# Optimization experiments

Measured on AMD Instinct MI355X. Metric: run time of the kernel, lower is better.

## Reference

```python
import jax, jax.numpy as jnp
import numpy as np
from jax import lax

DIM, HEADS, DIM_HEAD = 768, 12, 64
INNER = HEADS * DIM_HEAD
DIM_ROT = 32
FH = FW = 32
N = 1 + FH * FW
B = 8


def setup_inputs() -> dict:
    key = jax.random.key(0)
    ks = jax.random.split(key, 8)
    s = 0.02
    return {
        "x": jax.random.normal(ks[0], (B, N, DIM), jnp.float32),
        "sin": jax.random.normal(ks[1], (N - 1, DIM_ROT), jnp.float32),
        "cos": jax.random.normal(ks[2], (N - 1, DIM_ROT), jnp.float32),
        "ln_g": jnp.ones((DIM,), jnp.float32),
        "ln_b": jnp.zeros((DIM,), jnp.float32),
        "dw_w": jax.random.normal(ks[3], (DIM, 1, 5, 5), jnp.float32) * s,
        "pw_w": jax.random.normal(ks[4], (INNER, DIM, 1, 1), jnp.float32) * s,
        "kv_w": jax.random.normal(ks[5], (DIM, 2 * INNER), jnp.float32) * s,
        "out_w": jax.random.normal(ks[6], (INNER, DIM), jnp.float32) * s,
        "out_b": jnp.zeros((DIM,), jnp.float32),
        "fmap_h": FH,
        "fmap_w": FW,
    }


def _rotate_every_two(t):
    # (..., d) with pairs (x1, x2) -> (-x2, x1)
    shp = t.shape
    t = t.reshape(*shp[:-1], -1, 2)
    x1, x2 = t[..., 0], t[..., 1]
    return jnp.stack((-x2, x1), axis=-1).reshape(shp)


def _layernorm(x, g, b, eps=1e-5):
    mu = jnp.mean(x, -1, keepdims=True)
    var = jnp.var(x, -1, keepdims=True)
    return (x - mu) * lax.rsqrt(var + eps) * g + b


def reference(x, sin, cos, ln_g, ln_b, dw_w, pw_w, kv_w, out_w, out_b, fmap_h, fmap_w):
    b, n, _ = x.shape
    scale = DIM_HEAD ** -0.5
    xn = _layernorm(x, ln_g, ln_b)

    # --- query path: SpatialConv (depthwise 5x5 + 1x1), cls via Identity ---
    cls_tok, spatial = xn[:, :1], xn[:, 1:]
    fmap = spatial.reshape(b, fmap_h, fmap_w, DIM).transpose(0, 3, 1, 2)  # NCHW
    fmap = lax.conv_general_dilated(
        fmap, dw_w, window_strides=(1, 1), padding=[(2, 2), (2, 2)],
        dimension_numbers=("NCHW", "OIHW", "NCHW"), feature_group_count=DIM)
    fmap = lax.conv_general_dilated(
        fmap, pw_w, window_strides=(1, 1), padding="VALID",
        dimension_numbers=("NCHW", "OIHW", "NCHW"))
    q = fmap.transpose(0, 2, 3, 1).reshape(b, fmap_h * fmap_w, INNER)
    q = jnp.concatenate((cls_tok, q), axis=1)  # cls_proj is Identity (dim==inner)

    # --- kv projection ---
    kv = xn @ kv_w
    k, v = kv[..., :INNER], kv[..., INNER:]

    def to_heads(t):  # b n (h d) -> (b h) n d
        return t.reshape(b, n, HEADS, DIM_HEAD).transpose(0, 2, 1, 3).reshape(b * HEADS, n, DIM_HEAD)

    q, k, v = map(to_heads, (q, k, v))

    # --- partial rotary, skipping cls token ---
    def apply_rot(t):
        t_cls, t_sp = t[:, :1], t[:, 1:]
        t_rot, t_pass = t_sp[..., :DIM_ROT], t_sp[..., DIM_ROT:]
        t_rot = t_rot * cos + _rotate_every_two(t_rot) * sin
        return jnp.concatenate((t_cls, jnp.concatenate((t_rot, t_pass), -1)), axis=1)

    q, k = apply_rot(q), apply_rot(k)

    dots = jnp.einsum("bid,bjd->bij", q, k) * scale
    attn = jax.nn.softmax(dots, axis=-1)
    out = jnp.einsum("bij,bjd->bid", attn, v)
    out = out.reshape(b, HEADS, n, DIM_HEAD).transpose(0, 2, 1, 3).reshape(b, n, INNER)
    return out @ out_w + out_b
```

## Files before the change

### kernel.cpp

```cpp
#include <hip/hip_runtime.h>
#include <cstddef>

#define NSEQ   1025
#define NBATCH 8
#define NTOK   8200
#define DIMX   768
#define NHEADS 12
#define DHEAD  64
#define VTP    1040
#define LDP    72
#define CP     136

typedef short bf16x8 __attribute__((ext_vector_type(8)));
typedef float f32x4  __attribute__((ext_vector_type(4)));
typedef unsigned short u16;

__device__ __forceinline__ float bf2f(u16 u) {
    unsigned v = (unsigned)u << 16; float f; __builtin_memcpy(&f, &v, 4); return f;
}
__device__ __forceinline__ u16 f2bf(float f) {
    unsigned u; __builtin_memcpy(&u, &f, 4);
    return (u16)((u + 0x7FFFu + ((u >> 16) & 1u)) >> 16);
}

__device__ __forceinline__ void gl2lds16(const u16* g, u16* l) {
    __builtin_amdgcn_global_load_lds((__attribute__((address_space(1))) void*)g,
                                     (__attribute__((address_space(3))) void*)l, 16, 0, 0);
}

__launch_bounds__(256)
__global__ void ln_kernel(const float* __restrict__ x, const float* __restrict__ g,
                          const float* __restrict__ bb, u16* __restrict__ xn,
                          u16* __restrict__ qout)
{
    int t = blockIdx.x, tid = threadIdx.x;
    const float* xp = x + (size_t)t * DIMX;
    float v0 = xp[tid], v1 = xp[tid + 256], v2 = xp[tid + 512];
    float s  = v0 + v1 + v2;
    float ss = v0*v0 + v1*v1 + v2*v2;
    for (int off = 32; off > 0; off >>= 1) {
        s  += __shfl_down(s,  off, 64);
        ss += __shfl_down(ss, off, 64);
    }
    __shared__ float red[8];
    __shared__ float stats[2];
    int w = tid >> 6, lane = tid & 63;
    if (lane == 0) { red[w] = s; red[4 + w] = ss; }
    __syncthreads();
    if (tid == 0) {
        float S  = red[0] + red[1] + red[2] + red[3];
        float SS = red[4] + red[5] + red[6] + red[7];
        float mu  = S * (1.0f / DIMX);
        float var = SS * (1.0f / DIMX) - mu * mu;
        stats[0] = mu; stats[1] = rsqrtf(var + 1e-5f);
    }
    __syncthreads();
    float mu = stats[0], rs = stats[1];
    float y0 = (v0 - mu) * rs * g[tid]       + bb[tid];
    float y1 = (v1 - mu) * rs * g[tid + 256] + bb[tid + 256];
    float y2 = (v2 - mu) * rs * g[tid + 512] + bb[tid + 512];
    u16* op = xn + (size_t)t * DIMX;
    op[tid] = f2bf(y0); op[tid + 256] = f2bf(y1); op[tid + 512] = f2bf(y2);
    int bq = t / NSEQ;
    if (t == bq * NSEQ) {
        int c0 = tid, c1 = tid + 256, c2 = tid + 512;
        qout[((size_t)(bq * NHEADS + (c0 >> 6)) * NSEQ) * DHEAD + (c0 & 63)] = f2bf(y0 * 0.125f);
        qout[((size_t)(bq * NHEADS + (c1 >> 6)) * NSEQ) * DHEAD + (c1 & 63)] = f2bf(y1 * 0.125f);
        qout[((size_t)(bq * NHEADS + (c2 >> 6)) * NSEQ) * DHEAD + (c2 & 63)] = f2bf(y2 * 0.125f);
    }
}

__launch_bounds__(256)
__global__ void preproc_kernel(const float* __restrict__ dw_w, const float* __restrict__ pw_w,
                               const float* __restrict__ kv_w, const float* __restrict__ out_w,
                               float* __restrict__ dwT, u16* __restrict__ pw_bf,
                               u16* __restrict__ kv_wT, u16* __restrict__ out_wT)
{
    __shared__ float tile[32][33];
    int blk = blockIdx.x, tid = threadIdx.x;
    if (blk < 75) {
        int idx = blk * 256 + tid;
        if (idx < 768 * 25) {
            int c = idx / 25, wi = idx % 25;
            dwT[wi * 768 + c] = dw_w[idx];
        }
        return;
    }
    if (blk < 2379) {
        int i = (blk - 75) * 256 + tid;
        pw_bf[i] = f2bf(pw_w[i]);
        return;
    }
    const float* in; u16* out; int R, C, bx, by;
    if (blk < 3531) {
        int t2 = blk - 2379; bx = t2 % 48; by = t2 / 48;
        in = kv_w; out = kv_wT; R = 768; C = 1536;
    } else {
        int t2 = blk - 3531; bx = t2 % 24; by = t2 / 24;
        in = out_w; out = out_wT; R = 768; C = 768;
    }
    int tx = tid & 31, ty = tid >> 5;
    int xg = bx * 32 + tx, y0 = by * 32;
    for (int i = ty; i < 32; i += 8)
        tile[i][tx] = in[(size_t)(y0 + i) * C + xg];
    __syncthreads();
    int xo = by * 32 + tx, yo0 = bx * 32;
    for (int i = ty; i < 32; i += 8)
        out[(size_t)(yo0 + i) * R + xo] = f2bf(tile[tx][i]);
}

__launch_bounds__(256)
__global__ void dw_kernel(const u16* __restrict__ xn, const float* __restrict__ wt,
                          u16* __restrict__ out)
{
    int gid = blockIdx.x * 256 + threadIdx.x;
    int pix = gid / 96, cg = gid - pix * 96;
    int c = cg * 8;
    int b = pix >> 10, p = pix & 1023, y = p >> 5, x0 = p & 31;
    float acc[8] = {};
    for (int dy = 0; dy < 5; dy++) {
        int yy = y + dy - 2;
        if ((unsigned)yy >= 32u) continue;
        for (int dx = 0; dx < 5; dx++) {
            int xx = x0 + dx - 2;
            if ((unsigned)xx >= 32u) continue;
            const u16* ip = xn + ((size_t)(b * NSEQ) + 1 + yy * 32 + xx) * DIMX + c;
            uint4 iv = *(const uint4*)ip;
            const float* wp = wt + (dy * 5 + dx) * DIMX + c;
            float4 w0 = *(const float4*)wp;
            float4 w1 = *(const float4*)(wp + 4);
            acc[0] += bf2f((u16)(iv.x & 0xFFFFu)) * w0.x;
            acc[1] += bf2f((u16)(iv.x >> 16))     * w0.y;
            acc[2] += bf2f((u16)(iv.y & 0xFFFFu)) * w0.z;
            acc[3] += bf2f((u16)(iv.y >> 16))     * w0.w;
            acc[4] += bf2f((u16)(iv.z & 0xFFFFu)) * w1.x;
            acc[5] += bf2f((u16)(iv.z >> 16))     * w1.y;
            acc[6] += bf2f((u16)(iv.w & 0xFFFFu)) * w1.z;
            acc[7] += bf2f((u16)(iv.w >> 16))     * w1.w;
        }
    }
    uint4 ov;
    ov.x = (unsigned)f2bf(acc[0]) | ((unsigned)f2bf(acc[1]) << 16);
    ov.y = (unsigned)f2bf(acc[2]) | ((unsigned)f2bf(acc[3]) << 16);
    ov.z = (unsigned)f2bf(acc[4]) | ((unsigned)f2bf(acc[5]) << 16);
    ov.w = (unsigned)f2bf(acc[6]) | ((unsigned)f2bf(acc[7]) << 16);
    *(uint4*)(out + (size_t)pix * DIMX + c) = ov;
}

template<int MODE>
__launch_bounds__(256)
__global__ void gemm_bf16(const u16* __restrict__ A, const u16* __restrict__ Bn,
                          const float* __restrict__ bias, u16* __restrict__ Ob0,
                          u16* __restrict__ Ob1, float* __restrict__ Of,
                          const float* __restrict__ sinb, const float* __restrict__ cosb,
                          int M)
{
    __shared__ u16 smem[128 * CP];
    u16* As = smem;
    u16* Bs = smem + 8192;
    const int tid  = threadIdx.x;
    const int wave = tid >> 6, lane = tid & 63;
    const int q8 = lane >> 4, cc = lane & 15;
    const int wr = wave >> 1, wc = wave & 1;
    const long r0 = (long)blockIdx.y * 128;
    const int  c0 = blockIdx.x * 128;

    f32x4 acc[4][4] = {};

    for (int k0 = 0; k0 < 768; k0 += 64) {
        __syncthreads();
        #pragma unroll
        for (int p = 0; p < 4; p++) {
            int chunk = wave * 256 + p * 64 + lane;
            int row = chunk >> 3, cs = chunk & 7;
            int src = cs ^ (row & 7);
            const u16* ga = A  + (size_t)(r0 + row) * 768 + k0 + src * 8;
            const u16* gb = Bn + (size_t)(c0 + row) * 768 + k0 + src * 8;
            u16* la = As + (size_t)(wave * 256 + p * 64) * 8;
            u16* lb = Bs + (size_t)(wave * 256 + p * 64) * 8;
            gl2lds16(ga, la);
            gl2lds16(gb, lb);
        }
        __syncthreads();
        #pragma unroll
        for (int ks = 0; ks < 2; ks++) {
            const int chsw = (((ks * 4 + q8) ^ (cc & 7)) * 8);
            bf16x8 af[4], bfr[4];
            #pragma unroll
            for (int mi = 0; mi < 4; mi++)
                af[mi] = *(const bf16x8*)(As + (wr * 64 + mi * 16 + cc) * 64 + chsw);
            #pragma unroll
            for (int ni = 0; ni < 4; ni++)
                bfr[ni] = *(const bf16x8*)(Bs + (wc * 64 + ni * 16 + cc) * 64 + chsw);
            #pragma unroll
            for (int mi = 0; mi < 4; mi++)
                #pragma unroll
                for (int ni = 0; ni < 4; ni++)
                    acc[mi][ni] = __builtin_amdgcn_mfma_f32_16x16x32_bf16(af[mi], bfr[ni], acc[mi][ni], 0, 0, 0);
        }
    }

    if (MODE == 2) {
        #pragma unroll
        for (int mi = 0; mi < 4; mi++) {
            #pragma unroll
            for (int r = 0; r < 4; r++) {
                long row = r0 + wr * 64 + mi * 16 + q8 * 4 + r;
                if (row >= M) continue;
                #pragma unroll
                for (int ni = 0; ni < 4; ni++) {
                    int col = c0 + wc * 64 + ni * 16 + cc;
                    Of[(size_t)row * 768 + col] = acc[mi][ni][r] + bias[col];
                }
            }
        }
        return;
    }

    __syncthreads();
    #pragma unroll
    for (int mi = 0; mi < 4; mi++)
        #pragma unroll
        for (int r = 0; r < 4; r++) {
            int lr = wr * 64 + mi * 16 + q8 * 4 + r;
            #pragma unroll
            for (int ni = 0; ni < 4; ni++)
                smem[lr * CP + wc * 64 + ni * 16 + cc] = f2bf(acc[mi][ni][r]);
        }
    __syncthreads();
    #pragma unroll
    for (int p = 0; p < 8; p++) {
        int id = p * 256 + tid;
        int row = id >> 4, c8 = (id & 15) * 8;
        long grow = r0 + row;
        if (grow >= M) continue;
        uint4 val = *(const uint4*)(smem + row * CP + c8);
        int b, n;
        if (MODE == 1) { b = (int)(grow >> 10); n = (int)(grow & 1023) + 1; }
        else           { b = (int)(grow / NSEQ); n = (int)(grow % NSEQ); }
        int col = c0 + c8;
        u16* dst; int c2;
        bool isV = (MODE == 0 && col >= 768);
        if (isV) { dst = Ob1; c2 = col - 768; }
        else     { dst = Ob0; c2 = col; }
        int d0 = c2 & 63;
        if (!isV) {
            u16 e[8];
            unsigned wv[4] = {val.x, val.y, val.z, val.w};
            #pragma unroll
            for (int j = 0; j < 4; j++) { e[2*j] = (u16)(wv[j] & 0xFFFFu); e[2*j+1] = (u16)(wv[j] >> 16); }
            bool doro = (d0 < 32) && (n >= 1);
            if (MODE == 1 || doro) {
                float f[8];
                #pragma unroll
                for (int j = 0; j < 8; j++) f[j] = bf2f(e[j]);
                if (MODE == 1) {
                    #pragma unroll
                    for (int j = 0; j < 8; j++) f[j] *= 0.125f;
                }
                if (doro) {
                    int pos = n - 1;
                    const float* cp = cosb + pos * 32 + d0;
                    const float* sp = sinb + pos * 32 + d0;
                    float4 cv0 = *(const float4*)cp, cv1 = *(const float4*)(cp + 4);
                    float4 sv0 = *(const float4*)sp, sv1 = *(const float4*)(sp + 4);
                    float ca[8] = {cv0.x, cv0.y, cv0.z, cv0.w, cv1.x, cv1.y, cv1.z, cv1.w};
                    float sa[8] = {sv0.x, sv0.y, sv0.z, sv0.w, sv1.x, sv1.y, sv1.z, sv1.w};
                    #pragma unroll
                    for (int pr = 0; pr < 4; pr++) {
                        float a = f[2*pr], bb2 = f[2*pr+1];
                        f[2*pr]   = a   * ca[2*pr]   - bb2 * sa[2*pr];
                        f[2*pr+1] = bb2 * ca[2*pr+1] + a   * sa[2*pr+1];
                    }
                }
                #pragma unroll
                for (int j = 0; j < 8; j++) e[j] = f2bf(f[j]);
            }
            #pragma unroll
            for (int j = 0; j < 4; j++) wv[j] = (unsigned)e[2*j] | ((unsigned)e[2*j+1] << 16);
            val = make_uint4(wv[0], wv[1], wv[2], wv[3]);
        }
        *(uint4*)(dst + ((size_t)(b * NHEADS + (c2 >> 6)) * NSEQ + n) * DHEAD + (c2 & 63)) = val;
    }
}

__global__ void vt_kernel(const u16* __restrict__ v, u16* __restrict__ Vt)
{
    __shared__ u16 tile[32][33];
    int bh = blockIdx.z;
    int n0 = blockIdx.x * 32, d0 = blockIdx.y * 32;
    for (int i = threadIdx.y; i < 32; i += 8) {
        int n = n0 + i;
        tile[i][threadIdx.x] = (n < NSEQ) ? v[((size_t)bh * NSEQ + n) * 64 + d0 + threadIdx.x] : (u16)0;
    }
    __syncthreads();
    for (int i = threadIdx.y; i < 32; i += 8) {
        int n = n0 + threadIdx.x;
        if (n < VTP) Vt[((size_t)bh * 64 + d0 + i) * VTP + n] = tile[threadIdx.x][i];
    }
}

__launch_bounds__(256)
__global__ void attn_kernel(const u16* __restrict__ q, const u16* __restrict__ k,
                            const u16* __restrict__ Vt, u16* __restrict__ o)
{
    __shared__ u16 Kb[2][64 * 64];
    __shared__ u16 Vb[2][64 * 64];
    __shared__ u16 Ps[4 * 16 * LDP];
    const int tid  = threadIdx.x;
    const int wave = tid >> 6, lane = tid & 63;
    const int q8 = lane >> 4, cc = lane & 15;
    const int bh = blockIdx.x;
    const int i0 = blockIdx.y * 64;
    const int b = bh / NHEADS, h = bh % NHEADS;
    const size_t kbase  = (size_t)bh * NSEQ * 64;
    const size_t vtbase = (size_t)bh * 64 * VTP;

    bf16x8 aq[2];
    {
        const u16* qp = q + kbase + (size_t)(i0 + wave * 16 + cc) * 64;
        aq[0] = *(const bf16x8*)(qp + q8 * 8);
        aq[1] = *(const bf16x8*)(qp + 32 + q8 * 8);
    }

    auto stage = [&](int jt, int buf) {
        int j0 = jt * 64;
        #pragma unroll
        for (int p = 0; p < 2; p++) {
            int chunk = wave * 128 + p * 64 + lane;
            int row = chunk >> 3, cs = chunk & 7;
            int src = cs ^ (row & 7);
            u16* kd = Kb[buf] + (size_t)(wave * 128 + p * 64) * 8;
            u16* vd = Vb[buf] + (size_t)(wave * 128 + p * 64) * 8;
            gl2lds16(k  + kbase  + (size_t)(j0 + row) * 64 + src * 8, kd);
            gl2lds16(Vt + vtbase + (size_t)row * VTP + j0 + src * 8, vd);
        }
    };

    stage(0, 0);
    f32x4 O[4] = {};
    float lsum[4] = {0.f, 0.f, 0.f, 0.f};
    u16* Psw = Ps + wave * 16 * LDP;

    for (int jt = 0; jt < 17; jt++) {
        __syncthreads();
        const u16* Kc = Kb[jt & 1];
        const u16* Vc = Vb[jt & 1];
        if (jt < 16) stage(jt + 1, (jt + 1) & 1);

        f32x4 sf[4] = {};
        #pragma unroll
        for (int ks = 0; ks < 2; ks++) {
            #pragma unroll
            for (int ni = 0; ni < 4; ni++) {
                bf16x8 bk = *(const bf16x8*)(Kc + (ni * 16 + cc) * 64 + (((ks * 4 + q8) ^ (cc & 7)) * 8));
                sf[ni] = __builtin_amdgcn_mfma_f32_16x16x32_bf16(aq[ks], bk, sf[ni], 0, 0, 0);
            }
        }

        bool mask = (jt == 16);
        #pragma unroll
        for (int ni = 0; ni < 4; ni++) {
            #pragma unroll
            for (int r = 0; r < 4; r++) {
                float p = __expf(sf[ni][r]);
                if (mask && (1024 + ni * 16 + cc >= NSEQ)) p = 0.f;
                lsum[r] += p;
                unsigned u; __builtin_memcpy(&u, &p, 4);
                Psw[(q8 * 4 + r) * LDP + ni * 16 + cc] = (u16)((u + 0x8000u) >> 16);
            }
        }

        #pragma unroll
        for (int ks = 0; ks < 2; ks++) {
            bf16x8 pa = *(const bf16x8*)(Psw + cc * LDP + ks * 32 + q8 * 8);
            #pragma unroll
            for (int ni = 0; ni < 4; ni++) {
                bf16x8 vb = *(const bf16x8*)(Vc + (ni * 16 + cc) * 64 + (((ks * 4 + q8) ^ (cc & 7)) * 8));
                O[ni] = __builtin_amdgcn_mfma_f32_16x16x32_bf16(pa, vb, O[ni], 0, 0, 0);
            }
        }
    }

    #pragma unroll
    for (int r = 0; r < 4; r++) {
        lsum[r] += __shfl_xor(lsum[r], 1, 64);
        lsum[r] += __shfl_xor(lsum[r], 2, 64);
        lsum[r] += __shfl_xor(lsum[r], 4, 64);
        lsum[r] += __shfl_xor(lsum[r], 8, 64);
    }
    #pragma unroll
    for (int r = 0; r < 4; r++) {
        int i = i0 + wave * 16 + q8 * 4 + r;
        if (i >= NSEQ) continue;
        float inv = 1.0f / lsum[r];
        #pragma unroll
        for (int ni = 0; ni < 4; ni++)
            o[((size_t)(b * NSEQ + i)) * 768 + h * 64 + ni * 16 + cc] = f2bf(O[ni][r] * inv);
    }
}

extern "C" void kernel_launch(void* const* d_in, const int* in_sizes, int n_in,
                              void* d_out, int out_size, void* d_ws, size_t ws_size,
                              hipStream_t stream)
{
    const float* x     = (const float*)d_in[0];
    const float* sinb  = (const float*)d_in[1];
    const float* cosb  = (const float*)d_in[2];
    const float* ln_g  = (const float*)d_in[3];
    const float* ln_b  = (const float*)d_in[4];
    const float* dw_w  = (const float*)d_in[5];
    const float* pw_w  = (const float*)d_in[6];
    const float* kv_w  = (const float*)d_in[7];
    const float* out_w = (const float*)d_in[8];
    const float* out_b = (const float*)d_in[9];
    (void)in_sizes; (void)n_in; (void)out_size; (void)ws_size;

    u16* ws = (u16*)d_ws;
    u16* xn_bf    = ws;
    u16* dwout_bf = ws + 6297600;
    u16* q_bf     = ws + 12589056;
    u16* k_bf     = ws + 18886656;
    u16* v_bf     = ws + 25184256;
    u16* Vt       = ws + 31481856;
    u16* pw_bf    = ws + 37871616;
    u16* kv_wT    = ws + 38461440;
    u16* out_wT   = ws + 39641088;
    float* dwT    = (float*)(ws + 40230912);
    u16* attn_bf  = xn_bf;

    ln_kernel      <<<NTOK, 256, 0, stream>>>(x, ln_g, ln_b, xn_bf, q_bf);
    preproc_kernel <<<4107, 256, 0, stream>>>(dw_w, pw_w, kv_w, out_w, dwT, pw_bf, kv_wT, out_wT);
    dw_kernel      <<<3072, 256, 0, stream>>>(xn_bf, dwT, dwout_bf);
    gemm_bf16<1>   <<<dim3(6, 64), 256, 0, stream>>>(dwout_bf, pw_bf, nullptr, q_bf, nullptr, nullptr, sinb, cosb, 8192);
    gemm_bf16<0>   <<<dim3(12, 65), 256, 0, stream>>>(xn_bf, kv_wT, nullptr, k_bf, v_bf, nullptr, sinb, cosb, NTOK);
    vt_kernel      <<<dim3(33, 2, 96), dim3(32, 8), 0, stream>>>(v_bf, Vt);
    attn_kernel    <<<dim3(96, 17), 256, 0, stream>>>(q_bf, k_bf, Vt, attn_bf);
    gemm_bf16<2>   <<<dim3(6, 65), 256, 0, stream>>>(attn_bf, out_wT, out_b, nullptr, nullptr, (float*)d_out, nullptr, nullptr, NTOK);
}
```

Baseline: 306.7 us.

## Merge Q and KV projection GEMMs into one launch; double attention query tile

The two projection GEMMs (KV from the normalized input, Q from the depthwise output) are merged into one kernel launch of 1164 blocks, with each block choosing its operands and mode from the block index. This removes a launch and the tail gap between them. The attention kernel now gives each wave 32 query rows instead of 16, so each loaded K/V tile feeds twice the MFMA work, and the grid shrinks from 17 to 9 row-blocks. In exchange the attention kernel uses more registers and LDS, which may lower occupancy, and the last row-block wastes more padded rows.

```diff
diff --git a/kernel.cpp b/kernel.cpp
--- a/kernel.cpp
+++ b/kernel.cpp
@@ -147,13 +147,12 @@
     *(uint4*)(out + (size_t)pix * DIMX + c) = ov;
 }
 
-template<int MODE>
 __launch_bounds__(256)
-__global__ void gemm_bf16(const u16* __restrict__ A, const u16* __restrict__ Bn,
-                          const float* __restrict__ bias, u16* __restrict__ Ob0,
-                          u16* __restrict__ Ob1, float* __restrict__ Of,
-                          const float* __restrict__ sinb, const float* __restrict__ cosb,
-                          int M)
+__global__ void gemm_proj(const u16* __restrict__ xn, const u16* __restrict__ dwout,
+                          const u16* __restrict__ kvB, const u16* __restrict__ pwB,
+                          u16* __restrict__ kOut, u16* __restrict__ vOut,
+                          u16* __restrict__ qOut,
+                          const float* __restrict__ sinb, const float* __restrict__ cosb)
 {
     __shared__ u16 smem[128 * CP];
     u16* As = smem;
@@ -162,8 +161,15 @@
     const int wave = tid >> 6, lane = tid & 63;
     const int q8 = lane >> 4, cc = lane & 15;
     const int wr = wave >> 1, wc = wave & 1;
-    const long r0 = (long)blockIdx.y * 128;
-    const int  c0 = blockIdx.x * 128;
+
+    int bid = blockIdx.x;
+    int mode, bx, M;
+    long r0;
+    const u16 *A, *Bn;
+    if (bid < 780) { mode = 0; bx = bid % 12; r0 = (long)(bid / 12) * 128; A = xn;    Bn = kvB; M = NTOK; }
+    else { int t2 = bid - 780; mode = 1; bx = t2 % 6; r0 = (long)(t2 / 6) * 128; A = dwout; Bn = pwB; M = 8192; }
+    const int c0 = bx * 128;
+    u16* Ob0 = (mode == 0) ? kOut : qOut;
 
     f32x4 acc[4][4] = {};
 
@@ -200,23 +206,6 @@
         }
     }
 
-    if (MODE == 2) {
-        #pragma unroll
-        for (int mi = 0; mi < 4; mi++) {
-            #pragma unroll
-            for (int r = 0; r < 4; r++) {
-                long row = r0 + wr * 64 + mi * 16 + q8 * 4 + r;
-                if (row >= M) continue;
-                #pragma unroll
-                for (int ni = 0; ni < 4; ni++) {
-                    int col = c0 + wc * 64 + ni * 16 + cc;
-                    Of[(size_t)row * 768 + col] = acc[mi][ni][r] + bias[col];
-                }
-            }
-        }
-        return;
-    }
-
     __syncthreads();
     #pragma unroll
     for (int mi = 0; mi < 4; mi++)
@@ -236,13 +225,13 @@
         if (grow >= M) continue;
         uint4 val = *(const uint4*)(smem + row * CP + c8);
         int b, n;
-        if (MODE == 1) { b = (int)(grow >> 10); n = (int)(grow & 1023) + 1; }
+        if (mode == 1) { b = (int)(grow >> 10); n = (int)(grow & 1023) + 1; }
         else           { b = (int)(grow / NSEQ); n = (int)(grow % NSEQ); }
         int col = c0 + c8;
         u16* dst; int c2;
-        bool isV = (MODE == 0 && col >= 768);
-        if (isV) { dst = Ob1; c2 = col - 768; }
-        else     { dst = Ob0; c2 = col; }
+        bool isV = (mode == 0 && col >= 768);
+        if (isV) { dst = vOut; c2 = col - 768; }
+        else     { dst = Ob0;  c2 = col; }
         int d0 = c2 & 63;
         if (!isV) {
             u16 e[8];
@@ -250,11 +239,11 @@
             #pragma unroll
             for (int j = 0; j < 4; j++) { e[2*j] = (u16)(wv[j] & 0xFFFFu); e[2*j+1] = (u16)(wv[j] >> 16); }
             bool doro = (d0 < 32) && (n >= 1);
-            if (MODE == 1 || doro) {
+            if (mode == 1 || doro) {
                 float f[8];
                 #pragma unroll
                 for (int j = 0; j < 8; j++) f[j] = bf2f(e[j]);
-                if (MODE == 1) {
+                if (mode == 1) {
                     #pragma unroll
                     for (int j = 0; j < 8; j++) f[j] *= 0.125f;
                 }
@@ -284,6 +273,69 @@
     }
 }
 
+__launch_bounds__(256)
+__global__ void gemm_out(const u16* __restrict__ A, const u16* __restrict__ Bn,
+                         const float* __restrict__ bias, float* __restrict__ Of, int M)
+{
+    __shared__ u16 smem[32768 / 2 * 2];
+    u16* As = smem;
+    u16* Bs = smem + 8192;
+    const int tid  = threadIdx.x;
+    const int wave = tid >> 6, lane = tid & 63;
+    const int q8 = lane >> 4, cc = lane & 15;
+    const int wr = wave >> 1, wc = wave & 1;
+    const long r0 = (long)blockIdx.y * 128;
+    const int  c0 = blockIdx.x * 128;
+
+    f32x4 acc[4][4] = {};
+
+    for (int k0 = 0; k0 < 768; k0 += 64) {
+        __syncthreads();
+        #pragma unroll
+        for (int p = 0; p < 4; p++) {
+            int chunk = wave * 256 + p * 64 + lane;
+            int row = chunk >> 3, cs = chunk & 7;
+            int src = cs ^ (row & 7);
+            const u16* ga = A  + (size_t)(r0 + row) * 768 + k0 + src * 8;
+            const u16* gb = Bn + (size_t)(c0 + row) * 768 + k0 + src * 8;
+            u16* la = As + (size_t)(wave * 256 + p * 64) * 8;
+            u16* lb = Bs + (size_t)(wave * 256 + p * 64) * 8;
+            gl2lds16(ga, la);
+            gl2lds16(gb, lb);
+        }
+        __syncthreads();
+        #pragma unroll
+        for (int ks = 0; ks < 2; ks++) {
+            const int chsw = (((ks * 4 + q8) ^ (cc & 7)) * 8);
+            bf16x8 af[4], bfr[4];
+            #pragma unroll
+            for (int mi = 0; mi < 4; mi++)
+                af[mi] = *(const bf16x8*)(As + (wr * 64 + mi * 16 + cc) * 64 + chsw);
+            #pragma unroll
+            for (int ni = 0; ni < 4; ni++)
+                bfr[ni] = *(const bf16x8*)(Bs + (wc * 64 + ni * 16 + cc) * 64 + chsw);
+            #pragma unroll
+            for (int mi = 0; mi < 4; mi++)
+                #pragma unroll
+                for (int ni = 0; ni < 4; ni++)
+                    acc[mi][ni] = __builtin_amdgcn_mfma_f32_16x16x32_bf16(af[mi], bfr[ni], acc[mi][ni], 0, 0, 0);
+        }
+    }
+    #pragma unroll
+    for (int mi = 0; mi < 4; mi++) {
+        #pragma unroll
+        for (int r = 0; r < 4; r++) {
+            long row = r0 + wr * 64 + mi * 16 + q8 * 4 + r;
+            if (row >= M) continue;
+            #pragma unroll
+            for (int ni = 0; ni < 4; ni++) {
+                int col = c0 + wc * 64 + ni * 16 + cc;
+                Of[(size_t)row * 768 + col] = acc[mi][ni][r] + bias[col];
+            }
+        }
+    }
+}
+
 __global__ void vt_kernel(const u16* __restrict__ v, u16* __restrict__ Vt)
 {
     __shared__ u16 tile[32][33];
@@ -306,21 +358,22 @@
 {
     __shared__ u16 Kb[2][64 * 64];
     __shared__ u16 Vb[2][64 * 64];
-    __shared__ u16 Ps[4 * 16 * LDP];
+    __shared__ u16 Ps[4 * 32 * LDP];
     const int tid  = threadIdx.x;
     const int wave = tid >> 6, lane = tid & 63;
     const int q8 = lane >> 4, cc = lane & 15;
     const int bh = blockIdx.x;
-    const int i0 = blockIdx.y * 64;
+    const int i0 = blockIdx.y * 128;
     const int b = bh / NHEADS, h = bh % NHEADS;
     const size_t kbase  = (size_t)bh * NSEQ * 64;
     const size_t vtbase = (size_t)bh * 64 * VTP;
 
-    bf16x8 aq[2];
-    {
-        const u16* qp = q + kbase + (size_t)(i0 + wave * 16 + cc) * 64;
-        aq[0] = *(const bf16x8*)(qp + q8 * 8);
-        aq[1] = *(const bf16x8*)(qp + 32 + q8 * 8);
+    bf16x8 aq[2][2];
+    #pragma unroll
+    for (int mi = 0; mi < 2; mi++) {
+        const u16* qp = q + kbase + (size_t)(i0 + wave * 32 + mi * 16 + cc) * 64;
+        aq[mi][0] = *(const bf16x8*)(qp + q8 * 8);
+        aq[mi][1] = *(const bf16x8*)(qp + 32 + q8 * 8);
     }
 
     auto stage = [&](int jt, int buf) {
@@ -338,9 +391,9 @@
     };
 
     stage(0, 0);
-    f32x4 O[4] = {};
-    float lsum[4] = {0.f, 0.f, 0.f, 0.f};
-    u16* Psw = Ps + wave * 16 * LDP;
+    f32x4 O[2][4] = {};
+    float lsum[2][4] = {};
+    u16* Psw = Ps + wave * 32 * LDP;
 
     for (int jt = 0; jt < 17; jt++) {
         __syncthreads();
@@ -348,56 +401,68 @@
         const u16* Vc = Vb[jt & 1];
         if (jt < 16) stage(jt + 1, (jt + 1) & 1);
 
-        f32x4 sf[4] = {};
+        f32x4 sf[2][4] = {};
         #pragma unroll
         for (int ks = 0; ks < 2; ks++) {
             #pragma unroll
             for (int ni = 0; ni < 4; ni++) {
                 bf16x8 bk = *(const bf16x8*)(Kc + (ni * 16 + cc) * 64 + (((ks * 4 + q8) ^ (cc & 7)) * 8));
-                sf[ni] = __builtin_amdgcn_mfma_f32_16x16x32_bf16(aq[ks], bk, sf[ni], 0, 0, 0);
+                #pragma unroll
+                for (int mi = 0; mi < 2; mi++)
+                    sf[mi][ni] = __builtin_amdgcn_mfma_f32_16x16x32_bf16(aq[mi][ks], bk, sf[mi][ni], 0, 0, 0);
             }
         }
 
         bool mask = (jt == 16);
         #pragma unroll
-        for (int ni = 0; ni < 4; ni++) {
-            #pragma unroll
-            for (int r = 0; r < 4; r++) {
-                float p = __expf(sf[ni][r]);
-                if (mask && (1024 + ni * 16 + cc >= NSEQ)) p = 0.f;
-                lsum[r] += p;
-                unsigned u; __builtin_memcpy(&u, &p, 4);
-                Psw[(q8 * 4 + r) * LDP + ni * 16 + cc] = (u16)((u + 0x8000u) >> 16);
-            }
-        }
+        for (int mi = 0; mi < 2; mi++)
+            #pragma unroll
+            for (int ni = 0; ni < 4; ni++)
+                #pragma unroll
+                for (int r = 0; r < 4; r++) {
+                    float p = __expf(sf[mi][ni][r]);
+                    if (mask && (1024 + ni * 16 + cc >= NSEQ)) p = 0.f;
+                    lsum[mi][r] += p;
+                    unsigned u; __builtin_memcpy(&u, &p, 4);
+                    Psw[(mi * 16 + q8 * 4 + r) * LDP + ni * 16 + cc] = (u16)((u + 0x8000u) >> 16);
+                }
 
         #pragma unroll
         for (int ks = 0; ks < 2; ks++) {
-            bf16x8 pa = *(const bf16x8*)(Psw + cc * LDP + ks * 32 + q8 * 8);
+            bf16x8 pa[2];
+            #pragma unroll
+            for (int mi = 0; mi < 2; mi++)
+                pa[mi] = *(const bf16x8*)(Psw + (mi * 16 + cc) * LDP + ks * 32 + q8 * 8);
             #pragma unroll
             for (int ni = 0; ni < 4; ni++) {
                 bf16x8 vb = *(const bf16x8*)(Vc + (ni * 16 + cc) * 64 + (((ks * 4 + q8) ^ (cc & 7)) * 8));
-                O[ni] = __builtin_amdgcn_mfma_f32_16x16x32_bf16(pa, vb, O[ni], 0, 0, 0);
+                #pragma unroll
+                for (int mi = 0; mi < 2; mi++)
+                    O[mi][ni] = __builtin_amdgcn_mfma_f32_16x16x32_bf16(pa[mi], vb, O[mi][ni], 0, 0, 0);
             }
         }
     }
 
     #pragma unroll
-    for (int r = 0; r < 4; r++) {
-        lsum[r] += __shfl_xor(lsum[r], 1, 64);
-        lsum[r] += __shfl_xor(lsum[r], 2, 64);
-        lsum[r] += __shfl_xor(lsum[r], 4, 64);
-        lsum[r] += __shfl_xor(lsum[r], 8, 64);
-    }
+    for (int mi = 0; mi < 2; mi++)
+        #pragma unroll
+        for (int r = 0; r < 4; r++) {
+            lsum[mi][r] += __shfl_xor(lsum[mi][r], 1, 64);
+            lsum[mi][r] += __shfl_xor(lsum[mi][r], 2, 64);
+            lsum[mi][r] += __shfl_xor(lsum[mi][r], 4, 64);
+            lsum[mi][r] += __shfl_xor(lsum[mi][r], 8, 64);
+        }
     #pragma unroll
-    for (int r = 0; r < 4; r++) {
-        int i = i0 + wave * 16 + q8 * 4 + r;
-        if (i >= NSEQ) continue;
-        float inv = 1.0f / lsum[r];
-        #pragma unroll
-        for (int ni = 0; ni < 4; ni++)
-            o[((size_t)(b * NSEQ + i)) * 768 + h * 64 + ni * 16 + cc] = f2bf(O[ni][r] * inv);
-    }
+    for (int mi = 0; mi < 2; mi++)
+        #pragma unroll
+        for (int r = 0; r < 4; r++) {
+            int i = i0 + wave * 32 + mi * 16 + q8 * 4 + r;
+            if (i >= NSEQ) continue;
+            float inv = 1.0f / lsum[mi][r];
+            #pragma unroll
+            for (int ni = 0; ni < 4; ni++)
+                o[((size_t)(b * NSEQ + i)) * 768 + h * 64 + ni * 16 + cc] = f2bf(O[mi][ni][r] * inv);
+        }
 }
 
 extern "C" void kernel_launch(void* const* d_in, const int* in_sizes, int n_in,
@@ -432,9 +497,8 @@
     ln_kernel      <<<NTOK, 256, 0, stream>>>(x, ln_g, ln_b, xn_bf, q_bf);
     preproc_kernel <<<4107, 256, 0, stream>>>(dw_w, pw_w, kv_w, out_w, dwT, pw_bf, kv_wT, out_wT);
     dw_kernel      <<<3072, 256, 0, stream>>>(xn_bf, dwT, dwout_bf);
-    gemm_bf16<1>   <<<dim3(6, 64), 256, 0, stream>>>(dwout_bf, pw_bf, nullptr, q_bf, nullptr, nullptr, sinb, cosb, 8192);
-    gemm_bf16<0>   <<<dim3(12, 65), 256, 0, stream>>>(xn_bf, kv_wT, nullptr, k_bf, v_bf, nullptr, sinb, cosb, NTOK);
+    gemm_proj      <<<1164, 256, 0, stream>>>(xn_bf, dwout_bf, kv_wT, pw_bf, k_bf, v_bf, q_bf, sinb, cosb);
     vt_kernel      <<<dim3(33, 2, 96), dim3(32, 8), 0, stream>>>(v_bf, Vt);
-    attn_kernel    <<<dim3(96, 17), 256, 0, stream>>>(q_bf, k_bf, Vt, attn_bf);
-    gemm_bf16<2>   <<<dim3(6, 65), 256, 0, stream>>>(attn_bf, out_wT, out_b, nullptr, nullptr, (float*)d_out, nullptr, nullptr, NTOK);
-}
+    attn_kernel    <<<dim3(96, 9), 256, 0, stream>>>(q_bf, k_bf, Vt, attn_bf);
+    gemm_out       <<<dim3(6, 65), 256, 0, stream>>>(attn_bf, out_wT, out_b, (float*)d_out, NTOK);
+}
```

After: 296.7 us. 1.03x faster.

## Fuse projection GEMMs, compute V transposed directly, and widen attention tiles

Applied to the files above, without the earlier changes.

Merges the layernorm and weight-preprocessing kernels into one launch, and merges the K, V and Q projection GEMMs into a single block-indexed kernel. V is now produced already transposed by swapping operands (kv weights as A, xn as B), so the separate transpose kernel and the intermediate V buffer are gone. The attention kernel moves to 512 threads covering 128 query rows per block, with a per-batch padded Vt stride of 1032. The aim is fewer launches, less global memory traffic, and less repeated K/V staging. In exchange, padded V columns read rows from the next batch or past the end of xn and depend on the tail mask for correctness, and the mask now hard-codes the 1025-token sequence length.

```diff
diff --git a/kernel.cpp b/kernel.cpp
--- a/kernel.cpp
+++ b/kernel.cpp
@@ -7,7 +7,7 @@
 #define DIMX   768
 #define NHEADS 12
 #define DHEAD  64
-#define VTP    1040
+#define VTP3   8320
 #define LDP    72
 #define CP     136
 
@@ -29,55 +29,55 @@
 }
 
 __launch_bounds__(256)
-__global__ void ln_kernel(const float* __restrict__ x, const float* __restrict__ g,
-                          const float* __restrict__ bb, u16* __restrict__ xn,
-                          u16* __restrict__ qout)
-{
-    int t = blockIdx.x, tid = threadIdx.x;
-    const float* xp = x + (size_t)t * DIMX;
-    float v0 = xp[tid], v1 = xp[tid + 256], v2 = xp[tid + 512];
-    float s  = v0 + v1 + v2;
-    float ss = v0*v0 + v1*v1 + v2*v2;
-    for (int off = 32; off > 0; off >>= 1) {
-        s  += __shfl_down(s,  off, 64);
-        ss += __shfl_down(ss, off, 64);
-    }
+__global__ void ln_pre_kernel(const float* __restrict__ x, const float* __restrict__ g,
+                              const float* __restrict__ bb, u16* __restrict__ xn,
+                              u16* __restrict__ qout,
+                              const float* __restrict__ dw_w, const float* __restrict__ pw_w,
+                              const float* __restrict__ kv_w, const float* __restrict__ out_w,
+                              float* __restrict__ dwT, u16* __restrict__ pw_bf,
+                              u16* __restrict__ kv_wT, u16* __restrict__ out_wT)
+{
     __shared__ float red[8];
     __shared__ float stats[2];
-    int w = tid >> 6, lane = tid & 63;
-    if (lane == 0) { red[w] = s; red[4 + w] = ss; }
-    __syncthreads();
-    if (tid == 0) {
-        float S  = red[0] + red[1] + red[2] + red[3];
-        float SS = red[4] + red[5] + red[6] + red[7];
-        float mu  = S * (1.0f / DIMX);
-        float var = SS * (1.0f / DIMX) - mu * mu;
-        stats[0] = mu; stats[1] = rsqrtf(var + 1e-5f);
-    }
-    __syncthreads();
-    float mu = stats[0], rs = stats[1];
-    float y0 = (v0 - mu) * rs * g[tid]       + bb[tid];
-    float y1 = (v1 - mu) * rs * g[tid + 256] + bb[tid + 256];
-    float y2 = (v2 - mu) * rs * g[tid + 512] + bb[tid + 512];
-    u16* op = xn + (size_t)t * DIMX;
-    op[tid] = f2bf(y0); op[tid + 256] = f2bf(y1); op[tid + 512] = f2bf(y2);
-    int bq = t / NSEQ;
-    if (t == bq * NSEQ) {
-        int c0 = tid, c1 = tid + 256, c2 = tid + 512;
-        qout[((size_t)(bq * NHEADS + (c0 >> 6)) * NSEQ) * DHEAD + (c0 & 63)] = f2bf(y0 * 0.125f);
-        qout[((size_t)(bq * NHEADS + (c1 >> 6)) * NSEQ) * DHEAD + (c1 & 63)] = f2bf(y1 * 0.125f);
-        qout[((size_t)(bq * NHEADS + (c2 >> 6)) * NSEQ) * DHEAD + (c2 & 63)] = f2bf(y2 * 0.125f);
-    }
-}
-
-__launch_bounds__(256)
-__global__ void preproc_kernel(const float* __restrict__ dw_w, const float* __restrict__ pw_w,
-                               const float* __restrict__ kv_w, const float* __restrict__ out_w,
-                               float* __restrict__ dwT, u16* __restrict__ pw_bf,
-                               u16* __restrict__ kv_wT, u16* __restrict__ out_wT)
-{
     __shared__ float tile[32][33];
-    int blk = blockIdx.x, tid = threadIdx.x;
+    int tid = threadIdx.x;
+    if (blockIdx.x < NTOK) {
+        int t = blockIdx.x;
+        const float* xp = x + (size_t)t * DIMX;
+        float v0 = xp[tid], v1 = xp[tid + 256], v2 = xp[tid + 512];
+        float s  = v0 + v1 + v2;
+        float ss = v0*v0 + v1*v1 + v2*v2;
+        for (int off = 32; off > 0; off >>= 1) {
+            s  += __shfl_down(s,  off, 64);
+            ss += __shfl_down(ss, off, 64);
+        }
+        int w = tid >> 6, lane = tid & 63;
+        if (lane == 0) { red[w] = s; red[4 + w] = ss; }
+        __syncthreads();
+        if (tid == 0) {
+            float S  = red[0] + red[1] + red[2] + red[3];
+            float SS = red[4] + red[5] + red[6] + red[7];
+            float mu  = S * (1.0f / DIMX);
+            float var = SS * (1.0f / DIMX) - mu * mu;
+            stats[0] = mu; stats[1] = rsqrtf(var + 1e-5f);
+        }
+        __syncthreads();
+        float mu = stats[0], rs = stats[1];
+        float y0 = (v0 - mu) * rs * g[tid]       + bb[tid];
+        float y1 = (v1 - mu) * rs * g[tid + 256] + bb[tid + 256];
+        float y2 = (v2 - mu) * rs * g[tid + 512] + bb[tid + 512];
+        u16* op = xn + (size_t)t * DIMX;
+        op[tid] = f2bf(y0); op[tid + 256] = f2bf(y1); op[tid + 512] = f2bf(y2);
+        int bq = t / NSEQ;
+        if (t == bq * NSEQ) {
+            int c0 = tid, c1 = tid + 256, c2 = tid + 512;
+            qout[((size_t)(bq * NHEADS + (c0 >> 6)) * NSEQ) * DHEAD + (c0 & 63)] = f2bf(y0 * 0.125f);
+            qout[((size_t)(bq * NHEADS + (c1 >> 6)) * NSEQ) * DHEAD + (c1 & 63)] = f2bf(y1 * 0.125f);
+            qout[((size_t)(bq * NHEADS + (c2 >> 6)) * NSEQ) * DHEAD + (c2 & 63)] = f2bf(y2 * 0.125f);
+        }
+        return;
+    }
+    int blk = blockIdx.x - NTOK;
     if (blk < 75) {
         int idx = blk * 256 + tid;
         if (idx < 768 * 25) {
@@ -147,13 +147,12 @@
     *(uint4*)(out + (size_t)pix * DIMX + c) = ov;
 }
 
-template<int MODE>
 __launch_bounds__(256)
-__global__ void gemm_bf16(const u16* __restrict__ A, const u16* __restrict__ Bn,
-                          const float* __restrict__ bias, u16* __restrict__ Ob0,
-                          u16* __restrict__ Ob1, float* __restrict__ Of,
-                          const float* __restrict__ sinb, const float* __restrict__ cosb,
-                          int M)
+__global__ void gemm_proj(const u16* __restrict__ xn, const u16* __restrict__ dwout,
+                          const u16* __restrict__ kvT, const u16* __restrict__ pwB,
+                          u16* __restrict__ kOut, u16* __restrict__ VtOut,
+                          u16* __restrict__ qOut,
+                          const float* __restrict__ sinb, const float* __restrict__ cosb)
 {
     __shared__ u16 smem[128 * CP];
     u16* As = smem;
@@ -162,8 +161,16 @@
     const int wave = tid >> 6, lane = tid & 63;
     const int q8 = lane >> 4, cc = lane & 15;
     const int wr = wave >> 1, wc = wave & 1;
-    const long r0 = (long)blockIdx.y * 128;
-    const int  c0 = blockIdx.x * 128;
+
+    int bid = blockIdx.x;
+    int mode, c0;
+    long r0;
+    const u16 *A, *Bn;
+    if (bid < 390)      { mode = 0; c0 = (bid % 6) * 128;  r0 = (long)(bid / 6) * 128;  A = xn;              Bn = kvT; }
+    else if (bid < 780) { int t2 = bid - 390;
+                          mode = 2; c0 = (t2 % 65) * 128;  r0 = (long)(t2 / 65) * 128; A = kvT + 768 * 768; Bn = xn; }
+    else                { int t2 = bid - 780;
+                          mode = 1; c0 = (t2 % 6) * 128;   r0 = (long)(t2 / 6) * 128;  A = dwout;           Bn = pwB; }
 
     f32x4 acc[4][4] = {};
 
@@ -174,8 +181,14 @@
             int chunk = wave * 256 + p * 64 + lane;
             int row = chunk >> 3, cs = chunk & 7;
             int src = cs ^ (row & 7);
+            long brow;
+            if (mode == 2) {
+                int s = c0 + row;
+                int bb2 = s / 1032;
+                brow = (long)bb2 * NSEQ + (s - bb2 * 1032);
+            } else brow = c0 + row;
             const u16* ga = A  + (size_t)(r0 + row) * 768 + k0 + src * 8;
-            const u16* gb = Bn + (size_t)(c0 + row) * 768 + k0 + src * 8;
+            const u16* gb = Bn + (size_t)brow * 768 + k0 + src * 8;
             u16* la = As + (size_t)(wave * 256 + p * 64) * 8;
             u16* lb = Bs + (size_t)(wave * 256 + p * 64) * 8;
             gl2lds16(ga, la);
@@ -200,23 +213,6 @@
         }
     }
 
-    if (MODE == 2) {
-        #pragma unroll
-        for (int mi = 0; mi < 4; mi++) {
-            #pragma unroll
-            for (int r = 0; r < 4; r++) {
-                long row = r0 + wr * 64 + mi * 16 + q8 * 4 + r;
-                if (row >= M) continue;
-                #pragma unroll
-                for (int ni = 0; ni < 4; ni++) {
-                    int col = c0 + wc * 64 + ni * 16 + cc;
-                    Of[(size_t)row * 768 + col] = acc[mi][ni][r] + bias[col];
-                }
-            }
-        }
-        return;
-    }
-
     __syncthreads();
     #pragma unroll
     for (int mi = 0; mi < 4; mi++)
@@ -228,33 +224,42 @@
                 smem[lr * CP + wc * 64 + ni * 16 + cc] = f2bf(acc[mi][ni][r]);
         }
     __syncthreads();
+
+    if (mode == 2) {
+        #pragma unroll
+        for (int p = 0; p < 8; p++) {
+            int id = p * 256 + tid;
+            int row = id >> 4, c8 = (id & 15) * 8;
+            uint4 val = *(const uint4*)(smem + row * CP + c8);
+            *(uint4*)(VtOut + (size_t)(r0 + row) * VTP3 + c0 + c8) = val;
+        }
+        return;
+    }
+
     #pragma unroll
     for (int p = 0; p < 8; p++) {
         int id = p * 256 + tid;
         int row = id >> 4, c8 = (id & 15) * 8;
         long grow = r0 + row;
-        if (grow >= M) continue;
+        if (grow >= ((mode == 1) ? 8192 : NTOK)) continue;
         uint4 val = *(const uint4*)(smem + row * CP + c8);
         int b, n;
-        if (MODE == 1) { b = (int)(grow >> 10); n = (int)(grow & 1023) + 1; }
+        if (mode == 1) { b = (int)(grow >> 10); n = (int)(grow & 1023) + 1; }
         else           { b = (int)(grow / NSEQ); n = (int)(grow % NSEQ); }
-        int col = c0 + c8;
-        u16* dst; int c2;
-        bool isV = (MODE == 0 && col >= 768);
-        if (isV) { dst = Ob1; c2 = col - 768; }
-        else     { dst = Ob0; c2 = col; }
+        int c2 = c0 + c8;
+        u16* dst = (mode == 1) ? qOut : kOut;
         int d0 = c2 & 63;
-        if (!isV) {
+        {
             u16 e[8];
             unsigned wv[4] = {val.x, val.y, val.z, val.w};
             #pragma unroll
             for (int j = 0; j < 4; j++) { e[2*j] = (u16)(wv[j] & 0xFFFFu); e[2*j+1] = (u16)(wv[j] >> 16); }
             bool doro = (d0 < 32) && (n >= 1);
-            if (MODE == 1 || doro) {
+            if (mode == 1 || doro) {
                 float f[8];
                 #pragma unroll
                 for (int j = 0; j < 8; j++) f[j] = bf2f(e[j]);
-                if (MODE == 1) {
+                if (mode == 1) {
                     #pragma unroll
                     for (int j = 0; j < 8; j++) f[j] *= 0.125f;
                 }
@@ -284,37 +289,84 @@
     }
 }
 
-__global__ void vt_kernel(const u16* __restrict__ v, u16* __restrict__ Vt)
-{
-    __shared__ u16 tile[32][33];
-    int bh = blockIdx.z;
-    int n0 = blockIdx.x * 32, d0 = blockIdx.y * 32;
-    for (int i = threadIdx.y; i < 32; i += 8) {
-        int n = n0 + i;
-        tile[i][threadIdx.x] = (n < NSEQ) ? v[((size_t)bh * NSEQ + n) * 64 + d0 + threadIdx.x] : (u16)0;
-    }
-    __syncthreads();
-    for (int i = threadIdx.y; i < 32; i += 8) {
-        int n = n0 + threadIdx.x;
-        if (n < VTP) Vt[((size_t)bh * 64 + d0 + i) * VTP + n] = tile[threadIdx.x][i];
-    }
-}
-
 __launch_bounds__(256)
+__global__ void gemm_out(const u16* __restrict__ A, const u16* __restrict__ Bn,
+                         const float* __restrict__ bias, float* __restrict__ Of, int M)
+{
+    __shared__ u16 smem[16384];
+    u16* As = smem;
+    u16* Bs = smem + 8192;
+    const int tid  = threadIdx.x;
+    const int wave = tid >> 6, lane = tid & 63;
+    const int q8 = lane >> 4, cc = lane & 15;
+    const int wr = wave >> 1, wc = wave & 1;
+    const long r0 = (long)blockIdx.y * 128;
+    const int  c0 = blockIdx.x * 128;
+
+    f32x4 acc[4][4] = {};
+
+    for (int k0 = 0; k0 < 768; k0 += 64) {
+        __syncthreads();
+        #pragma unroll
+        for (int p = 0; p < 4; p++) {
+            int chunk = wave * 256 + p * 64 + lane;
+            int row = chunk >> 3, cs = chunk & 7;
+            int src = cs ^ (row & 7);
+            const u16* ga = A  + (size_t)(r0 + row) * 768 + k0 + src * 8;
+            const u16* gb = Bn + (size_t)(c0 + row) * 768 + k0 + src * 8;
+            u16* la = As + (size_t)(wave * 256 + p * 64) * 8;
+            u16* lb = Bs + (size_t)(wave * 256 + p * 64) * 8;
+            gl2lds16(ga, la);
+            gl2lds16(gb, lb);
+        }
+        __syncthreads();
+        #pragma unroll
+        for (int ks = 0; ks < 2; ks++) {
+            const int chsw = (((ks * 4 + q8) ^ (cc & 7)) * 8);
+            bf16x8 af[4], bfr[4];
+            #pragma unroll
+            for (int mi = 0; mi < 4; mi++)
+                af[mi] = *(const bf16x8*)(As + (wr * 64 + mi * 16 + cc) * 64 + chsw);
+            #pragma unroll
+            for (int ni = 0; ni < 4; ni++)
+                bfr[ni] = *(const bf16x8*)(Bs + (wc * 64 + ni * 16 + cc) * 64 + chsw);
+            #pragma unroll
+            for (int mi = 0; mi < 4; mi++)
+                #pragma unroll
+                for (int ni = 0; ni < 4; ni++)
+                    acc[mi][ni] = __builtin_amdgcn_mfma_f32_16x16x32_bf16(af[mi], bfr[ni], acc[mi][ni], 0, 0, 0);
+        }
+    }
+    #pragma unroll
+    for (int mi = 0; mi < 4; mi++) {
+        #pragma unroll
+        for (int r = 0; r < 4; r++) {
+            long row = r0 + wr * 64 + mi * 16 + q8 * 4 + r;
+            if (row >= M) continue;
+            #pragma unroll
+            for (int ni = 0; ni < 4; ni++) {
+                int col = c0 + wc * 64 + ni * 16 + cc;
+                Of[(size_t)row * 768 + col] = acc[mi][ni][r] + bias[col];
+            }
+        }
+    }
+}
+
+__launch_bounds__(512)
 __global__ void attn_kernel(const u16* __restrict__ q, const u16* __restrict__ k,
                             const u16* __restrict__ Vt, u16* __restrict__ o)
 {
-    __shared__ u16 Kb[2][64 * 64];
-    __shared__ u16 Vb[2][64 * 64];
-    __shared__ u16 Ps[4 * 16 * LDP];
+    __shared__ u16 Kb[2][4096];
+    __shared__ u16 Vb[2][4096];
+    __shared__ u16 Ps[8 * 16 * LDP];
     const int tid  = threadIdx.x;
     const int wave = tid >> 6, lane = tid & 63;
     const int q8 = lane >> 4, cc = lane & 15;
     const int bh = blockIdx.x;
-    const int i0 = blockIdx.y * 64;
+    const int i0 = blockIdx.y * 128;
     const int b = bh / NHEADS, h = bh % NHEADS;
-    const size_t kbase  = (size_t)bh * NSEQ * 64;
-    const size_t vtbase = (size_t)bh * 64 * VTP;
+    const size_t kbase = (size_t)bh * NSEQ * 64;
+    const size_t vbase = (size_t)(h * 64) * VTP3 + (size_t)b * 1032;
 
     bf16x8 aq[2];
     {
@@ -325,16 +377,11 @@
 
     auto stage = [&](int jt, int buf) {
         int j0 = jt * 64;
-        #pragma unroll
-        for (int p = 0; p < 2; p++) {
-            int chunk = wave * 128 + p * 64 + lane;
-            int row = chunk >> 3, cs = chunk & 7;
-            int src = cs ^ (row & 7);
-            u16* kd = Kb[buf] + (size_t)(wave * 128 + p * 64) * 8;
-            u16* vd = Vb[buf] + (size_t)(wave * 128 + p * 64) * 8;
-            gl2lds16(k  + kbase  + (size_t)(j0 + row) * 64 + src * 8, kd);
-            gl2lds16(Vt + vtbase + (size_t)row * VTP + j0 + src * 8, vd);
-        }
+        int chunk = wave * 64 + lane;
+        int row = chunk >> 3, cs = chunk & 7;
+        int src = cs ^ (row & 7);
+        gl2lds16(k  + kbase + (size_t)(j0 + row) * 64 + src * 8, Kb[buf] + wave * 512);
+        gl2lds16(Vt + vbase + (size_t)row * VTP3 + j0 + src * 8,  Vb[buf] + wave * 512);
     };
 
     stage(0, 0);
@@ -360,16 +407,15 @@
 
         bool mask = (jt == 16);
         #pragma unroll
-        for (int ni = 0; ni < 4; ni++) {
+        for (int ni = 0; ni < 4; ni++)
             #pragma unroll
             for (int r = 0; r < 4; r++) {
                 float p = __expf(sf[ni][r]);
-                if (mask && (1024 + ni * 16 + cc >= NSEQ)) p = 0.f;
+                if (mask && (ni * 16 + cc != 0)) p = 0.f;
                 lsum[r] += p;
                 unsigned u; __builtin_memcpy(&u, &p, 4);
                 Psw[(q8 * 4 + r) * LDP + ni * 16 + cc] = (u16)((u + 0x8000u) >> 16);
             }
-        }
 
         #pragma unroll
         for (int ks = 0; ks < 2; ks++) {
@@ -421,20 +467,19 @@
     u16* dwout_bf = ws + 6297600;
     u16* q_bf     = ws + 12589056;
     u16* k_bf     = ws + 18886656;
-    u16* v_bf     = ws + 25184256;
-    u16* Vt       = ws + 31481856;
-    u16* pw_bf    = ws + 37871616;
-    u16* kv_wT    = ws + 38461440;
-    u16* out_wT   = ws + 39641088;
-    float* dwT    = (float*)(ws + 40230912);
+    u16* Vt       = ws + 25184256;
+    u16* pw_bf    = ws + 31574016;
+    u16* kv_wT    = ws + 32163840;
+    u16* out_wT   = ws + 33343488;
+    float* dwT    = (float*)(ws + 33933312);
     u16* attn_bf  = xn_bf;
 
-    ln_kernel      <<<NTOK, 256, 0, stream>>>(x, ln_g, ln_b, xn_bf, q_bf);
-    preproc_kernel <<<4107, 256, 0, stream>>>(dw_w, pw_w, kv_w, out_w, dwT, pw_bf, kv_wT, out_wT);
-    dw_kernel      <<<3072, 256, 0, stream>>>(xn_bf, dwT, dwout_bf);
-    gemm_bf16<1>   <<<dim3(6, 64), 256, 0, stream>>>(dwout_bf, pw_bf, nullptr, q_bf, nullptr, nullptr, sinb, cosb, 8192);
-    gemm_bf16<0>   <<<dim3(12, 65), 256, 0, stream>>>(xn_bf, kv_wT, nullptr, k_bf, v_bf, nullptr, sinb, cosb, NTOK);
-    vt_kernel      <<<dim3(33, 2, 96), dim3(32, 8), 0, stream>>>(v_bf, Vt);
-    attn_kernel    <<<dim3(96, 17), 256, 0, stream>>>(q_bf, k_bf, Vt, attn_bf);
-    gemm_bf16<2>   <<<dim3(6, 65), 256, 0, stream>>>(attn_bf, out_wT, out_b, nullptr, nullptr, (float*)d_out, nullptr, nullptr, NTOK);
-}
+    ln_pre_kernel <<<NTOK + 4107, 256, 0, stream>>>(x, ln_g, ln_b, xn_bf, q_bf,
+                                                    dw_w, pw_w, kv_w, out_w,
+                                                    dwT, pw_bf, kv_wT, out_wT);
+    dw_kernel     <<<3072, 256, 0, stream>>>(xn_bf, dwT, dwout_bf);
+    gemm_proj     <<<1164, 256, 0, stream>>>(xn_bf, dwout_bf, kv_wT, pw_bf,
+                                             k_bf, Vt, q_bf, sinb, cosb);
+    attn_kernel   <<<dim3(96, 9), 512, 0, stream>>>(q_bf, k_bf, Vt, attn_bf);
+    gemm_out      <<<dim3(6, 65), 256, 0, stream>>>(attn_bf, out_wT, out_b, (float*)d_out, NTOK);
+}
```

Measured after the change: 274.3 us. -10.6%, faster.
